# Optimization experiments

Measured on AMD Instinct MI355X. Metric: run time of the kernel, lower is better.

## Reference

```python
import jax, jax.numpy as jnp
import numpy as np

D_MODEL = 1024
NUM_HEADS = 16
HEAD_DIM = D_MODEL // NUM_HEADS  # 64
ROPE_THETA = 10000.0
SEQ_LEN = 4096
BATCH = 1


def apply_rope(x, positions, theta=ROPE_THETA):
    # x: [b, h, s, d], positions: [s]
    d = x.shape[-1]
    inv_freq = theta ** (-jnp.arange(0, d, 2, dtype=jnp.float32) / d)  # [d/2]
    angles = positions.astype(jnp.float32)[:, None] * inv_freq[None, :]  # [s, d/2]
    cos = jnp.cos(angles)  # [s, d/2]
    sin = jnp.sin(angles)
    x1 = x[..., 0::2]  # [b, h, s, d/2]
    x2 = x[..., 1::2]
    r1 = x1 * cos - x2 * sin
    r2 = x1 * sin + x2 * cos
    # interleave back to [..., d]
    out = jnp.stack([r1, r2], axis=-1).reshape(x.shape)
    return out.astype(x.dtype)


def setup_inputs() -> dict:
    key = jax.random.key(0)
    k_x, k_qkv, k_o = jax.random.split(key, 3)
    scale_in = 1.0 / np.sqrt(D_MODEL)
    return {
        "x": jax.random.normal(k_x, (BATCH, SEQ_LEN, D_MODEL), dtype=jnp.float32),
        "token_positions": jnp.arange(SEQ_LEN, dtype=jnp.int64 if jax.config.jax_enable_x64 else jnp.int32),
        "w_qkv": jax.random.normal(k_qkv, (3 * D_MODEL, D_MODEL), dtype=jnp.float32) * scale_in,
        "w_o": jax.random.normal(k_o, (D_MODEL, D_MODEL), dtype=jnp.float32) * scale_in,
    }


def reference(x, token_positions, w_qkv, w_o):
    b, s, _ = x.shape
    # QKV projection (Linear without bias, weight [out, in])
    x_qkv = jnp.einsum('bsd,ed->bse', x, w_qkv)  # [b, s, 3*d_model]
    # rearrange 'b s (three heads kv) -> three b heads s kv'
    x_qkv = x_qkv.reshape(b, s, 3, NUM_HEADS, HEAD_DIM)
    x_qkv = jnp.transpose(x_qkv, (2, 0, 3, 1, 4))  # [3, b, h, s, d]
    q, k, v = x_qkv[0], x_qkv[1], x_qkv[2]
    q = apply_rope(q, token_positions)
    k = apply_rope(k, token_positions)
    # scaled dot-product attention with causal mask
    scores = jnp.einsum('bhnd,bhmd->bhnm', q, k) / jnp.sqrt(jnp.float32(HEAD_DIM))
    causal = jnp.tril(jnp.ones((s, s), dtype=bool))  # [s, s]
    scores = jnp.where(causal[None, None], scores, jnp.float32(-jnp.inf))
    weights = jax.nn.softmax(scores, axis=-1)
    attn = jnp.einsum('bhnm,bhmd->bhnd', weights, v)  # [b, h, s, d]
    attn = jnp.transpose(attn, (0, 2, 1, 3)).reshape(b, s, NUM_HEADS * HEAD_DIM)
    return jnp.einsum('bsd,ed->bse', attn, w_o)
```

## Files before the change

kernel.cpp:

```cpp
#include <hip/hip_runtime.h>

#define SEQ 4096
#define DMODEL 1024
#define HEADS 16
#define HD 64
#define NQKV 3072

typedef __attribute__((ext_vector_type(8))) __bf16 bf16x8;
typedef __attribute__((ext_vector_type(4))) __bf16 bf16x4;
typedef __attribute__((ext_vector_type(8))) short short8;
typedef __attribute__((ext_vector_type(4))) float f32x4;
typedef __attribute__((ext_vector_type(16))) float f32x16;
typedef __attribute__((ext_vector_type(4))) unsigned int u32x4;

__device__ __forceinline__ unsigned short f2bf(float f) {
    unsigned u = __builtin_bit_cast(unsigned, f);
    return (unsigned short)((u + 0x7fffu + ((u >> 16) & 1u)) >> 16);
}
__device__ __forceinline__ float bf2f(unsigned short h) {
    return __builtin_bit_cast(float, (unsigned)h << 16);
}
__device__ __forceinline__ unsigned cvt_pk_bf16(float lo, float hi) {
    unsigned r;
    asm("v_cvt_pk_bf16_f32 %0, %1, %2" : "=v"(r) : "v"(lo), "v"(hi));
    return r;
}

__device__ __forceinline__ void gload16(const void* g, void* l) {
    __builtin_amdgcn_global_load_lds(
        (const __attribute__((address_space(1))) unsigned int*)g,
        (__attribute__((address_space(3))) unsigned int*)l, 16, 0, 0);
}

#define TS(qt, kh) (0x40 | ((kh) << 5) | (qt))
__device__ __constant__ unsigned char TASKS[48] = {
    TS(31,0), TS(31,1), TS(30,0), 15,
    TS(30,1), TS(29,0), TS(29,1), TS(28,0), 14,
    TS(28,1), TS(27,0), TS(27,1), TS(26,0), 13,
    TS(26,1), TS(25,0), TS(25,1), TS(24,0), 12,
    TS(24,1), TS(23,0), TS(23,1), TS(22,0), 11,
    TS(22,1), TS(21,0), TS(21,1), TS(20,0), 10,
    TS(20,1), TS(19,0), TS(19,1), TS(18,0), 9,
    TS(18,1), TS(17,0), TS(17,1), TS(16,0), 8,
    TS(16,1), 7,
    6, 5, 4, 3, 2, 1, 0
};

__global__ void f2bf_all(const float* __restrict__ x, const float* __restrict__ wqkv,
                         const float* __restrict__ wo, unsigned short* __restrict__ dst) {
    const int N0 = SEQ * DMODEL / 4;
    const int N1 = N0 + NQKV * DMODEL / 4;
    const int NT = N1 + DMODEL * DMODEL / 4;
    int i = blockIdx.x * 256 + threadIdx.x;
    int stride = gridDim.x * 256;
    for (; i < NT; i += stride) {
        const float4* src;
        if (i < N0)      src = reinterpret_cast<const float4*>(x) + i;
        else if (i < N1) src = reinterpret_cast<const float4*>(wqkv) + (i - N0);
        else             src = reinterpret_cast<const float4*>(wo) + (i - N1);
        float4 f = *src;
        ushort4 o;
        o.x = f2bf(f.x); o.y = f2bf(f.y); o.z = f2bf(f.z); o.w = f2bf(f.w);
        reinterpret_cast<ushort4*>(dst)[i] = o;
    }
}

template <int EPI>
__global__ __launch_bounds__(256) void gemm_bt(const unsigned short* __restrict__ A,
                                               const unsigned short* __restrict__ B,
                                               float* __restrict__ outF,
                                               unsigned short* __restrict__ outB,
                                               int M, int N, int K) {
    alignas(16) __shared__ unsigned short a_lds[2][128 * 32];
    alignas(16) __shared__ unsigned short b_lds[2][128 * 32];
    const int tid = threadIdx.x;
    const int wave = tid >> 6, lane = tid & 63;
    const int l16 = lane & 15, g = lane >> 4;
    const int wr = wave >> 1, wc = wave & 1;
    const int bm = blockIdx.x, bn = blockIdx.y;

    const int lrow = lane >> 2;
    const int lcol = (lane & 3) * 8;

    const unsigned short* Ag = A + (size_t)(bm * 128 + lrow) * K + lcol;
    const unsigned short* Bg = B + (size_t)(bn * 128 + lrow) * K + lcol;

    f32x4 acc[4][4] = {};
    const int NS = K / 32;

    auto STAGE = [&](int b, int ks) {
#pragma unroll
        for (int j = 0; j < 2; ++j) {
            int chunk = wave * 2 + j;
            gload16(Ag + (size_t)(chunk * 16) * K + ks * 32, a_lds[b] + chunk * 512);
            gload16(Bg + (size_t)(chunk * 16) * K + ks * 32, b_lds[b] + chunk * 512);
        }
    };

    STAGE(0, 0);

    for (int ks = 0; ks < NS; ++ks) {
        const int cur = ks & 1;
        asm volatile("s_waitcnt vmcnt(0)" ::: "memory");
        __builtin_amdgcn_s_barrier();
        if (ks + 1 < NS) STAGE(cur ^ 1, ks + 1);

        bf16x8 af[4], bfr[4];
#pragma unroll
        for (int m = 0; m < 4; ++m)
            af[m] = *reinterpret_cast<const bf16x8*>(a_lds[cur] + (wr * 64 + m * 16 + l16) * 32 + g * 8);
#pragma unroll
        for (int n = 0; n < 4; ++n)
            bfr[n] = *reinterpret_cast<const bf16x8*>(b_lds[cur] + (wc * 64 + n * 16 + l16) * 32 + g * 8);
        __builtin_amdgcn_s_setprio(1);
#pragma unroll
        for (int m = 0; m < 4; ++m)
#pragma unroll
            for (int n = 0; n < 4; ++n)
                acc[m][n] = __builtin_amdgcn_mfma_f32_16x16x32_bf16(af[m], bfr[n], acc[m][n], 0, 0, 0);
        __builtin_amdgcn_s_setprio(0);
    }

#pragma unroll
    for (int m = 0; m < 4; ++m)
#pragma unroll
        for (int n = 0; n < 4; ++n)
#pragma unroll
            for (int r = 0; r < 4; ++r) {
                int row = bm * 128 + wr * 64 + m * 16 + g * 4 + r;
                int col = bn * 128 + wc * 64 + n * 16 + l16;
                float v = acc[m][n][r];
                if (EPI == 0) {
                    int part = col >> 10;
                    int hd = col & 1023;
                    int h = hd >> 6, d = hd & 63;
                    outB[(size_t)((part * HEADS + h) * SEQ + row) * HD + d] = f2bf(v);
                } else {
                    outF[(size_t)row * N + col] = v;
                }
            }
}

__global__ __launch_bounds__(256) void rope_kernel(unsigned short* qkv, const int* __restrict__ pos) {
    int idx = blockIdx.x * 256 + threadIdx.x;
    int chunk = idx & 7;
    int row = idx >> 3;
    int s = row & (SEQ - 1);
    int ph = row >> 12;
    float p = (float)pos[s];
    float scale = (ph < HEADS) ? 0.125f * 1.4426950408889634f : 1.0f;
    unsigned short* base = qkv + ((size_t)ph * SEQ + s) * HD + chunk * 8;
    short8 v = *reinterpret_cast<short8*>(base);
    short8 o;
    const float k = -13.287712379549449f / 32.0f;
#pragma unroll
    for (int j = 0; j < 4; ++j) {
        int i = chunk * 4 + j;
        float ang = p * exp2f((float)i * k);
        float sn, cs;
        sincosf(ang, &sn, &cs);
        float x1 = bf2f((unsigned short)v[2 * j]);
        float x2 = bf2f((unsigned short)v[2 * j + 1]);
        o[2 * j]     = (short)f2bf((x1 * cs - x2 * sn) * scale);
        o[2 * j + 1] = (short)f2bf((x1 * sn + x2 * cs) * scale);
    }
    *reinterpret_cast<short8*>(base) = o;
}

__global__ __launch_bounds__(256) void transpose_v(const unsigned short* __restrict__ qkv,
                                                   unsigned short* __restrict__ vt) {
    const int st = blockIdx.x;
    const int h = blockIdx.y;
    __shared__ unsigned short tile[64][72];
    const unsigned short* Vg = qkv + (size_t)((2 * HEADS + h) * SEQ) * HD;
    const int tid = threadIdx.x;
#pragma unroll
    for (int j = 0; j < 2; ++j) {
        int b = (tid + j * 256) * 8;
        int row = b >> 6;
        int col = b & 63;
        short8 v = *reinterpret_cast<const short8*>(Vg + (size_t)(st * 64 + row) * HD + col);
#pragma unroll
        for (int i = 0; i < 8; ++i) tile[row][col + i] = (unsigned short)v[i];
    }
    __syncthreads();
#pragma unroll
    for (int j = 0; j < 2; ++j) {
        int b = (tid + j * 256) * 8;
        int d = b >> 6;
        int sc = b & 63;
        short8 o;
#pragma unroll
        for (int i = 0; i < 8; ++i) o[i] = (short)tile[sc + i][d];
        *reinterpret_cast<short8*>(vt + (size_t)(h * HD + d) * SEQ + st * 64 + sc) = o;
    }
}

__global__ __launch_bounds__(256) void attn_kernel(const unsigned short* __restrict__ qkv,
                                                   const unsigned short* __restrict__ vt,
                                                   unsigned short* __restrict__ attnout,
                                                   unsigned short* __restrict__ pO,
                                                   float* __restrict__ lmf) {
    const int bid = blockIdx.x;
    const int xcd = bid & 7;
    const int slot = bid >> 3;
    const int hloc = slot & 1;
    const unsigned char e = TASKS[slot >> 1];
    const int qtile = e & 31;
    const int khalf = (e >> 5) & 1;
    const bool isSplit = (e >> 6) != 0;
    const int T = qtile + 1, Hh = (T + 1) >> 1;
    const int k0 = isSplit ? (khalf ? Hh : 0) : 0;
    const int k1 = isSplit ? (khalf ? T : Hh) : T;
    const int h = xcd * 2 + hloc;

    const int tid = threadIdx.x;
    const int wave = tid >> 6, lane = tid & 63;
    const int l32 = lane & 31, hi = lane >> 5;

    alignas(16) __shared__ unsigned short k_lds[2][128 * 64];
    alignas(16) __shared__ unsigned short v_lds[2][2][64 * 64];

    const unsigned short* Qg = qkv + (size_t)((0 * HEADS + h) * SEQ) * HD;
    const unsigned short* Kg = qkv + (size_t)((1 * HEADS + h) * SEQ) * HD;
    const unsigned short* VTg = vt + (size_t)h * HD * SEQ;

    const int qbase = qtile * 128 + wave * 32;
    const int qrow = qbase + l32;

    bf16x8 qf[4];
#pragma unroll
    for (int dg = 0; dg < 4; ++dg)
        qf[dg] = *reinterpret_cast<const bf16x8*>(Qg + (size_t)qrow * HD + dg * 16 + hi * 8);

    f32x16 oa[2] = {};
    float m_r = -1e30f, l_r = 0.f;

    const int rsw = (l32 & 7) << 4;

    auto STAGE = [&](int b, int kt) {
#pragma unroll
        for (int i = 0; i < 4; ++i) {
            int base = wave * 4096 + i * 1024;
            int byte = base + lane * 16;
            int krow = byte >> 7;
            int kc8 = ((byte >> 4) & 7) ^ (krow & 7);
            gload16(Kg + (size_t)(kt * 128 + krow) * HD + kc8 * 8, (char*)k_lds[b] + base);
            int fr = byte >> 7;
            int h64 = fr >> 6, vd = fr & 63;
            int vc8 = ((byte >> 4) & 7) ^ (vd & 7);
            gload16(VTg + (size_t)vd * SEQ + kt * 128 + h64 * 64 + vc8 * 8,
                    (char*)v_lds[b] + base);
        }
    };

    STAGE(0, k0);

    for (int kt = k0; kt < k1; ++kt) {
        const int cur = (kt - k0) & 1;
        asm volatile("s_waitcnt vmcnt(0)" ::: "memory");
        __builtin_amdgcn_s_barrier();
        if (kt + 1 < k1) STAGE(cur ^ 1, kt + 1);

#pragma unroll
        for (int hh = 0; hh < 2; ++hh) {
            if (hh && (kt * 128 + 64) > (qbase + 31)) break;

            f32x16 s[2] = {};
            __builtin_amdgcn_s_setprio(1);
#pragma unroll
            for (int g = 0; g < 2; ++g) {
                int row = hh * 64 + g * 32 + l32;
#pragma unroll
                for (int dg = 0; dg < 4; ++dg) {
                    bf16x8 kf = *reinterpret_cast<const bf16x8*>(
                        (char*)k_lds[cur] + row * 128 + ((dg * 32 + hi * 16) ^ rsw));
                    s[g] = __builtin_amdgcn_mfma_f32_32x32x16_bf16(kf, qf[dg], s[g], 0, 0, 0);
                }
            }
            __builtin_amdgcn_s_setprio(0);

            if (kt * 128 + hh * 64 + 63 > qbase) {
#pragma unroll
                for (int g = 0; g < 2; ++g)
#pragma unroll
                    for (int r = 0; r < 16; ++r) {
                        int kv = kt * 128 + hh * 64 + g * 32 + (r & 3) + 8 * (r >> 2) + 4 * hi;
                        if (kv > qrow) s[g][r] = -1e30f;
                    }
            }

            float ma = -1e30f, mb = -1e30f, mc = -1e30f, md = -1e30f;
#pragma unroll
            for (int r = 0; r < 16; r += 4) {
                ma = fmaxf(ma, fmaxf(s[0][r], s[1][r]));
                mb = fmaxf(mb, fmaxf(s[0][r + 1], s[1][r + 1]));
                mc = fmaxf(mc, fmaxf(s[0][r + 2], s[1][r + 2]));
                md = fmaxf(md, fmaxf(s[0][r + 3], s[1][r + 3]));
            }
            float mx = fmaxf(fmaxf(ma, mb), fmaxf(mc, md));
            mx = fmaxf(mx, __shfl_xor(mx, 32));

            if (__any(mx > m_r + 8.0f)) {
                float mnew = fmaxf(m_r, mx);
                float alpha = __builtin_amdgcn_exp2f(m_r - mnew);
                m_r = mnew;
#pragma unroll
                for (int r = 0; r < 16; ++r) { oa[0][r] *= alpha; oa[1][r] *= alpha; }
                l_r *= alpha;
            }

#pragma unroll
            for (int g = 0; g < 2; ++g)
#pragma unroll
                for (int r = 0; r < 16; ++r) s[g][r] = __builtin_amdgcn_exp2f(s[g][r] - m_r);

            float ra = 0.f, rb = 0.f;
#pragma unroll
            for (int r = 0; r < 16; r += 2) {
                ra += s[0][r] + s[1][r];
                rb += s[0][r + 1] + s[1][r + 1];
            }
            float rs = ra + rb;
            rs += __shfl_xor(rs, 32);
            l_r += rs;

            __builtin_amdgcn_s_setprio(1);
#pragma unroll
            for (int g = 0; g < 2; ++g) {
                u32x4 pfw[2];
#pragma unroll
                for (int u = 0; u < 2; ++u) {
                    unsigned wA = cvt_pk_bf16(s[g][8 * u + 0], s[g][8 * u + 1]);
                    unsigned wC = cvt_pk_bf16(s[g][8 * u + 2], s[g][8 * u + 3]);
                    unsigned wB = cvt_pk_bf16(s[g][8 * u + 4], s[g][8 * u + 5]);
                    unsigned wD = cvt_pk_bf16(s[g][8 * u + 6], s[g][8 * u + 7]);
                    unsigned wAx = __shfl_xor((int)wA, 32), wBx = __shfl_xor((int)wB, 32);
                    unsigned wCx = __shfl_xor((int)wC, 32), wDx = __shfl_xor((int)wD, 32);
                    pfw[u][0] = hi ? wBx : wA;
                    pfw[u][1] = hi ? wDx : wC;
                    pfw[u][2] = hi ? wB : wAx;
                    pfw[u][3] = hi ? wD : wCx;
                }
#pragma unroll
                for (int u = 0; u < 2; ++u) {
                    bf16x8 pf = __builtin_bit_cast(bf16x8, pfw[u]);
                    int ks = g * 2 + u;
#pragma unroll
                    for (int dg = 0; dg < 2; ++dg) {
                        bf16x8 vf = *reinterpret_cast<const bf16x8*>(
                            (char*)v_lds[cur][hh] + (dg * 32 + l32) * 128 + ((ks * 32 + hi * 16) ^ rsw));
                        oa[dg] = __builtin_amdgcn_mfma_f32_32x32x16_bf16(vf, pf, oa[dg], 0, 0, 0);
                    }
                }
            }
            __builtin_amdgcn_s_setprio(0);
        }
    }

    const int ql = wave * 32 + l32;
    if (isSplit) {
        int sidx = (h * 16 + (qtile - 16)) * 2 + khalf;
        unsigned short* Op = pO + (size_t)sidx * 8192;
#pragma unroll
        for (int dg = 0; dg < 2; ++dg)
#pragma unroll
            for (int rq = 0; rq < 4; ++rq) {
                ushort4 ov;
                ov.x = f2bf(oa[dg][4 * rq + 0]);
                ov.y = f2bf(oa[dg][4 * rq + 1]);
                ov.z = f2bf(oa[dg][4 * rq + 2]);
                ov.w = f2bf(oa[dg][4 * rq + 3]);
                *reinterpret_cast<ushort4*>(Op + ql * 64 + dg * 32 + 8 * rq + 4 * hi) = ov;
            }
        if (hi == 0) {
            lmf[sidx * 256 + ql] = l_r;
            lmf[sidx * 256 + 128 + ql] = m_r;
        }
    } else {
        float inv = 1.0f / l_r;
        unsigned short* orow = attnout + (size_t)(qtile * 128 + ql) * DMODEL + h * HD;
#pragma unroll
        for (int dg = 0; dg < 2; ++dg)
#pragma unroll
            for (int rq = 0; rq < 4; ++rq) {
                ushort4 ov;
                ov.x = f2bf(oa[dg][4 * rq + 0] * inv);
                ov.y = f2bf(oa[dg][4 * rq + 1] * inv);
                ov.z = f2bf(oa[dg][4 * rq + 2] * inv);
                ov.w = f2bf(oa[dg][4 * rq + 3] * inv);
                *reinterpret_cast<ushort4*>(orow + dg * 32 + 8 * rq + 4 * hi) = ov;
            }
    }
}

__global__ __launch_bounds__(256) void merge_kernel(const unsigned short* __restrict__ pO,
                                                    const float* __restrict__ lmf,
                                                    unsigned short* __restrict__ attnout) {
    int idx = blockIdx.x * 256 + threadIdx.x;
    if (idx >= 16 * 16 * 1024) return;
    int h = idx / (16 * 1024);
    int r = idx % (16 * 1024);
    int qt = r >> 10;
    int rr = r & 1023;
    int q = rr >> 3, d8 = rr & 7;

    int s0 = (h * 16 + qt) * 2;
    float l0 = lmf[s0 * 256 + q],       m0 = lmf[s0 * 256 + 128 + q];
    float l1 = lmf[(s0 + 1) * 256 + q], m1 = lmf[(s0 + 1) * 256 + 128 + q];
    float m = fmaxf(m0, m1);
    float a0 = __builtin_amdgcn_exp2f(m0 - m), a1 = __builtin_amdgcn_exp2f(m1 - m);
    float L = l0 * a0 + l1 * a1;
    float c0 = a0 / L, c1 = a1 / L;

    const unsigned short* O0 = pO + (size_t)s0 * 8192 + q * 64 + d8 * 8;
    const unsigned short* O1 = O0 + 8192;
    short8 v0 = *reinterpret_cast<const short8*>(O0);
    short8 v1 = *reinterpret_cast<const short8*>(O1);
    short8 o;
#pragma unroll
    for (int j = 0; j < 8; ++j) {
        float val = bf2f((unsigned short)v0[j]) * c0 + bf2f((unsigned short)v1[j]) * c1;
        o[j] = (short)f2bf(val);
    }
    int qtile = qt + 16;
    *reinterpret_cast<short8*>(attnout + (size_t)(qtile * 128 + q) * DMODEL + h * HD + d8 * 8) = o;
}

extern "C" void kernel_launch(void* const* d_in, const int* in_sizes, int n_in,
                              void* d_out, int out_size, void* d_ws, size_t ws_size,
                              hipStream_t stream) {
    const float* x = (const float*)d_in[0];
    const int* pos = (const int*)d_in[1];
    const float* wqkv = (const float*)d_in[2];
    const float* wo = (const float*)d_in[3];
    float* out = (float*)d_out;

    unsigned short* xb = (unsigned short*)d_ws;
    unsigned short* wqkvb = xb + (size_t)SEQ * DMODEL;
    unsigned short* wob = wqkvb + (size_t)NQKV * DMODEL;
    unsigned short* qkvp = wob + (size_t)DMODEL * DMODEL;
    unsigned short* vt = qkvp + (size_t)3 * HEADS * SEQ * HD;
    unsigned short* attnb = vt + (size_t)HEADS * HD * SEQ;

    char* sbase = (char*)d_ws;
    float* lmf = (float*)sbase;
    unsigned short* pO = (unsigned short*)(sbase + (1 << 20));

    f2bf_all<<<2048, 256, 0, stream>>>(x, wqkv, wo, xb);

    dim3 g1(SEQ / 128, NQKV / 128);
    gemm_bt<0><<<g1, 256, 0, stream>>>(xb, wqkvb, nullptr, qkvp, SEQ, NQKV, DMODEL);

    rope_kernel<<<(2 * HEADS * SEQ * 8) / 256, 256, 0, stream>>>(qkvp, pos);
    transpose_v<<<dim3(SEQ / 64, HEADS), 256, 0, stream>>>(qkvp, vt);

    attn_kernel<<<768, 256, 0, stream>>>(qkvp, vt, attnb, pO, lmf);
    merge_kernel<<<(16 * 16 * 1024 + 255) / 256, 256, 0, stream>>>(pO, lmf, attnb);

    dim3 g2(SEQ / 128, DMODEL / 128);
    gemm_bt<1><<<g2, 256, 0, stream>>>(attnb, wob, out, nullptr, SEQ, DMODEL, DMODEL);
}
```

Before: 158.0 us.

## Use 256-row query tiles with persistent atomic work queue per XCD in attention

The attention kernel moves from 128-row query tiles with 256 threads to 256-row tiles with 512 threads (8 waves). The static one-block-per-task grid becomes persistent blocks that pull tasks from a per-XCD atomic counter, with a new split/unsplit task table and a matching merge kernel. The intent is better load balance across the causal triangle and more K/V reuse per staged tile, at the cost of extra barriers per task, a memset launch, and higher register/LDS pressure per block.

```diff
diff --git a/kernel.cpp b/kernel.cpp
--- a/kernel.cpp
+++ b/kernel.cpp
@@ -33,17 +33,12 @@
 }
 
 #define TS(qt, kh) (0x40 | ((kh) << 5) | (qt))
-__device__ __constant__ unsigned char TASKS[48] = {
-    TS(31,0), TS(31,1), TS(30,0), 15,
-    TS(30,1), TS(29,0), TS(29,1), TS(28,0), 14,
-    TS(28,1), TS(27,0), TS(27,1), TS(26,0), 13,
-    TS(26,1), TS(25,0), TS(25,1), TS(24,0), 12,
-    TS(24,1), TS(23,0), TS(23,1), TS(22,0), 11,
-    TS(22,1), TS(21,0), TS(21,1), TS(20,0), 10,
-    TS(20,1), TS(19,0), TS(19,1), TS(18,0), 9,
-    TS(18,1), TS(17,0), TS(17,1), TS(16,0), 8,
-    TS(16,1), 7,
-    6, 5, 4, 3, 2, 1, 0
+__device__ __constant__ unsigned char TASKS[28] = {
+    TS(15,0), TS(15,1), TS(14,0), TS(14,1), TS(13,0), TS(13,1),
+    TS(12,0), TS(12,1), TS(11,0), TS(11,1), TS(10,0), TS(10,1),
+    TS(9,0),  TS(9,1),  TS(8,0),  TS(8,1),  TS(7,0),  TS(7,1),
+    3,        TS(6,0),  TS(6,1),  2,        TS(5,0),  TS(5,1),
+    TS(4,0),  TS(4,1),  1,        0
 };
 
 __global__ void f2bf_all(const float* __restrict__ x, const float* __restrict__ wqkv,
@@ -196,201 +191,209 @@
     }
 }
 
-__global__ __launch_bounds__(256) void attn_kernel(const unsigned short* __restrict__ qkv,
+__global__ __launch_bounds__(512) void attn_kernel(const unsigned short* __restrict__ qkv,
                                                    const unsigned short* __restrict__ vt,
                                                    unsigned short* __restrict__ attnout,
+                                                   int* __restrict__ qcnt,
                                                    unsigned short* __restrict__ pO,
                                                    float* __restrict__ lmf) {
-    const int bid = blockIdx.x;
-    const int xcd = bid & 7;
-    const int slot = bid >> 3;
-    const int hloc = slot & 1;
-    const unsigned char e = TASKS[slot >> 1];
-    const int qtile = e & 31;
-    const int khalf = (e >> 5) & 1;
-    const bool isSplit = (e >> 6) != 0;
-    const int T = qtile + 1, Hh = (T + 1) >> 1;
-    const int k0 = isSplit ? (khalf ? Hh : 0) : 0;
-    const int k1 = isSplit ? (khalf ? T : Hh) : T;
-    const int h = xcd * 2 + hloc;
-
+    const int xcd = blockIdx.x & 7;
     const int tid = threadIdx.x;
     const int wave = tid >> 6, lane = tid & 63;
     const int l32 = lane & 31, hi = lane >> 5;
 
     alignas(16) __shared__ unsigned short k_lds[2][128 * 64];
     alignas(16) __shared__ unsigned short v_lds[2][2][64 * 64];
-
-    const unsigned short* Qg = qkv + (size_t)((0 * HEADS + h) * SEQ) * HD;
-    const unsigned short* Kg = qkv + (size_t)((1 * HEADS + h) * SEQ) * HD;
-    const unsigned short* VTg = vt + (size_t)h * HD * SEQ;
-
-    const int qbase = qtile * 128 + wave * 32;
-    const int qrow = qbase + l32;
-
-    bf16x8 qf[4];
-#pragma unroll
-    for (int dg = 0; dg < 4; ++dg)
-        qf[dg] = *reinterpret_cast<const bf16x8*>(Qg + (size_t)qrow * HD + dg * 16 + hi * 8);
-
-    f32x16 oa[2] = {};
-    float m_r = -1e30f, l_r = 0.f;
+    __shared__ int slot_sh;
 
     const int rsw = (l32 & 7) << 4;
 
-    auto STAGE = [&](int b, int kt) {
-#pragma unroll
-        for (int i = 0; i < 4; ++i) {
-            int base = wave * 4096 + i * 1024;
-            int byte = base + lane * 16;
-            int krow = byte >> 7;
-            int kc8 = ((byte >> 4) & 7) ^ (krow & 7);
-            gload16(Kg + (size_t)(kt * 128 + krow) * HD + kc8 * 8, (char*)k_lds[b] + base);
-            int fr = byte >> 7;
-            int h64 = fr >> 6, vd = fr & 63;
-            int vc8 = ((byte >> 4) & 7) ^ (vd & 7);
-            gload16(VTg + (size_t)vd * SEQ + kt * 128 + h64 * 64 + vc8 * 8,
-                    (char*)v_lds[b] + base);
+    for (;;) {
+        if (tid == 0) slot_sh = atomicAdd(&qcnt[xcd], 1);
+        __syncthreads();
+        const int t = slot_sh;
+        __syncthreads();
+        if (t >= 56) break;
+
+        const int hloc = t & 1;
+        const unsigned char e = TASKS[t >> 1];
+        const int qtile = e & 31;
+        const int khalf = (e >> 5) & 1;
+        const bool isSplit = (e >> 6) != 0;
+        const int T = 2 * qtile + 2, Hh = qtile + 1;
+        const int k0 = isSplit ? (khalf ? Hh : 0) : 0;
+        const int k1 = isSplit ? (khalf ? T : Hh) : T;
+        const int h = xcd * 2 + hloc;
+
+        const unsigned short* Qg = qkv + (size_t)((0 * HEADS + h) * SEQ) * HD;
+        const unsigned short* Kg = qkv + (size_t)((1 * HEADS + h) * SEQ) * HD;
+        const unsigned short* VTg = vt + (size_t)h * HD * SEQ;
+
+        const int qbase = qtile * 256 + wave * 32;
+        const int qrow = qbase + l32;
+
+        bf16x8 qf[4];
+#pragma unroll
+        for (int dg = 0; dg < 4; ++dg)
+            qf[dg] = *reinterpret_cast<const bf16x8*>(Qg + (size_t)qrow * HD + dg * 16 + hi * 8);
+
+        f32x16 oa[2] = {};
+        float m_r = -1e30f, l_r = 0.f;
+
+        auto STAGE = [&](int b, int kt) {
+#pragma unroll
+            for (int i = 0; i < 2; ++i) {
+                int base = wave * 2048 + i * 1024;
+                int byte = base + lane * 16;
+                int krow = byte >> 7;
+                int kc8 = ((byte >> 4) & 7) ^ (krow & 7);
+                gload16(Kg + (size_t)(kt * 128 + krow) * HD + kc8 * 8, (char*)k_lds[b] + base);
+                int fr = byte >> 7;
+                int h64 = fr >> 6, vd = fr & 63;
+                int vc8 = ((byte >> 4) & 7) ^ (vd & 7);
+                gload16(VTg + (size_t)vd * SEQ + kt * 128 + h64 * 64 + vc8 * 8,
+                        (char*)v_lds[b] + base);
+            }
+        };
+
+        STAGE(0, k0);
+
+        for (int kt = k0; kt < k1; ++kt) {
+            const int cur = (kt - k0) & 1;
+            asm volatile("s_waitcnt vmcnt(0)" ::: "memory");
+            __builtin_amdgcn_s_barrier();
+            if (kt + 1 < k1) STAGE(cur ^ 1, kt + 1);
+
+#pragma unroll
+            for (int hh = 0; hh < 2; ++hh) {
+                if (hh && (kt * 128 + 64) > (qbase + 31)) break;
+
+                f32x16 s[2] = {};
+                __builtin_amdgcn_s_setprio(1);
+#pragma unroll
+                for (int g = 0; g < 2; ++g) {
+                    int row = hh * 64 + g * 32 + l32;
+#pragma unroll
+                    for (int dg = 0; dg < 4; ++dg) {
+                        bf16x8 kf = *reinterpret_cast<const bf16x8*>(
+                            (char*)k_lds[cur] + row * 128 + ((dg * 32 + hi * 16) ^ rsw));
+                        s[g] = __builtin_amdgcn_mfma_f32_32x32x16_bf16(kf, qf[dg], s[g], 0, 0, 0);
+                    }
+                }
+                __builtin_amdgcn_s_setprio(0);
+
+                if (kt * 128 + hh * 64 + 63 > qbase) {
+#pragma unroll
+                    for (int g = 0; g < 2; ++g)
+#pragma unroll
+                        for (int r = 0; r < 16; ++r) {
+                            int kv = kt * 128 + hh * 64 + g * 32 + (r & 3) + 8 * (r >> 2) + 4 * hi;
+                            if (kv > qrow) s[g][r] = -1e30f;
+                        }
+                }
+
+                float ma = -1e30f, mb = -1e30f, mc = -1e30f, md = -1e30f;
+#pragma unroll
+                for (int r = 0; r < 16; r += 4) {
+                    ma = fmaxf(ma, fmaxf(s[0][r], s[1][r]));
+                    mb = fmaxf(mb, fmaxf(s[0][r + 1], s[1][r + 1]));
+                    mc = fmaxf(mc, fmaxf(s[0][r + 2], s[1][r + 2]));
+                    md = fmaxf(md, fmaxf(s[0][r + 3], s[1][r + 3]));
+                }
+                float mx = fmaxf(fmaxf(ma, mb), fmaxf(mc, md));
+                mx = fmaxf(mx, __shfl_xor(mx, 32));
+
+                if (__any(mx > m_r + 8.0f)) {
+                    float mnew = fmaxf(m_r, mx);
+                    float alpha = __builtin_amdgcn_exp2f(m_r - mnew);
+                    m_r = mnew;
+#pragma unroll
+                    for (int r = 0; r < 16; ++r) { oa[0][r] *= alpha; oa[1][r] *= alpha; }
+                    l_r *= alpha;
+                }
+
+#pragma unroll
+                for (int g = 0; g < 2; ++g)
+#pragma unroll
+                    for (int r = 0; r < 16; ++r) s[g][r] = __builtin_amdgcn_exp2f(s[g][r] - m_r);
+
+                float ra = 0.f, rb = 0.f;
+#pragma unroll
+                for (int r = 0; r < 16; r += 2) {
+                    ra += s[0][r] + s[1][r];
+                    rb += s[0][r + 1] + s[1][r + 1];
+                }
+                float rs = ra + rb;
+                rs += __shfl_xor(rs, 32);
+                l_r += rs;
+
+                __builtin_amdgcn_s_setprio(1);
+#pragma unroll
+                for (int g = 0; g < 2; ++g) {
+                    u32x4 pfw[2];
+#pragma unroll
+                    for (int u = 0; u < 2; ++u) {
+                        unsigned wA = cvt_pk_bf16(s[g][8 * u + 0], s[g][8 * u + 1]);
+                        unsigned wC = cvt_pk_bf16(s[g][8 * u + 2], s[g][8 * u + 3]);
+                        unsigned wB = cvt_pk_bf16(s[g][8 * u + 4], s[g][8 * u + 5]);
+                        unsigned wD = cvt_pk_bf16(s[g][8 * u + 6], s[g][8 * u + 7]);
+                        unsigned wAx = __shfl_xor((int)wA, 32), wBx = __shfl_xor((int)wB, 32);
+                        unsigned wCx = __shfl_xor((int)wC, 32), wDx = __shfl_xor((int)wD, 32);
+                        pfw[u][0] = hi ? wBx : wA;
+                        pfw[u][1] = hi ? wDx : wC;
+                        pfw[u][2] = hi ? wB : wAx;
+                        pfw[u][3] = hi ? wD : wCx;
+                    }
+#pragma unroll
+                    for (int u = 0; u < 2; ++u) {
+                        bf16x8 pf = __builtin_bit_cast(bf16x8, pfw[u]);
+                        int ks = g * 2 + u;
+#pragma unroll
+                        for (int dg = 0; dg < 2; ++dg) {
+                            bf16x8 vf = *reinterpret_cast<const bf16x8*>(
+                                (char*)v_lds[cur][hh] + (dg * 32 + l32) * 128 + ((ks * 32 + hi * 16) ^ rsw));
+                            oa[dg] = __builtin_amdgcn_mfma_f32_32x32x16_bf16(vf, pf, oa[dg], 0, 0, 0);
+                        }
+                    }
+                }
+                __builtin_amdgcn_s_setprio(0);
+            }
         }
-    };
-
-    STAGE(0, k0);
-
-    for (int kt = k0; kt < k1; ++kt) {
-        const int cur = (kt - k0) & 1;
-        asm volatile("s_waitcnt vmcnt(0)" ::: "memory");
-        __builtin_amdgcn_s_barrier();
-        if (kt + 1 < k1) STAGE(cur ^ 1, kt + 1);
-
-#pragma unroll
-        for (int hh = 0; hh < 2; ++hh) {
-            if (hh && (kt * 128 + 64) > (qbase + 31)) break;
-
-            f32x16 s[2] = {};
-            __builtin_amdgcn_s_setprio(1);
-#pragma unroll
-            for (int g = 0; g < 2; ++g) {
-                int row = hh * 64 + g * 32 + l32;
-#pragma unroll
-                for (int dg = 0; dg < 4; ++dg) {
-                    bf16x8 kf = *reinterpret_cast<const bf16x8*>(
-                        (char*)k_lds[cur] + row * 128 + ((dg * 32 + hi * 16) ^ rsw));
-                    s[g] = __builtin_amdgcn_mfma_f32_32x32x16_bf16(kf, qf[dg], s[g], 0, 0, 0);
-                }
+
+        const int ql = wave * 32 + l32;
+        if (isSplit) {
+            int sidx = (h * 12 + (qtile - 4)) * 2 + khalf;
+            unsigned short* Op = pO + (size_t)sidx * 16384;
+#pragma unroll
+            for (int dg = 0; dg < 2; ++dg)
+#pragma unroll
+                for (int rq = 0; rq < 4; ++rq) {
+                    ushort4 ov;
+                    ov.x = f2bf(oa[dg][4 * rq + 0]);
+                    ov.y = f2bf(oa[dg][4 * rq + 1]);
+                    ov.z = f2bf(oa[dg][4 * rq + 2]);
+                    ov.w = f2bf(oa[dg][4 * rq + 3]);
+                    *reinterpret_cast<ushort4*>(Op + ql * 64 + dg * 32 + 8 * rq + 4 * hi) = ov;
+                }
+            if (hi == 0) {
+                lmf[sidx * 512 + ql] = l_r;
+                lmf[sidx * 512 + 256 + ql] = m_r;
             }
-            __builtin_amdgcn_s_setprio(0);
-
-            if (kt * 128 + hh * 64 + 63 > qbase) {
-#pragma unroll
-                for (int g = 0; g < 2; ++g)
-#pragma unroll
-                    for (int r = 0; r < 16; ++r) {
-                        int kv = kt * 128 + hh * 64 + g * 32 + (r & 3) + 8 * (r >> 2) + 4 * hi;
-                        if (kv > qrow) s[g][r] = -1e30f;
-                    }
-            }
-
-            float ma = -1e30f, mb = -1e30f, mc = -1e30f, md = -1e30f;
-#pragma unroll
-            for (int r = 0; r < 16; r += 4) {
-                ma = fmaxf(ma, fmaxf(s[0][r], s[1][r]));
-                mb = fmaxf(mb, fmaxf(s[0][r + 1], s[1][r + 1]));
-                mc = fmaxf(mc, fmaxf(s[0][r + 2], s[1][r + 2]));
-                md = fmaxf(md, fmaxf(s[0][r + 3], s[1][r + 3]));
-            }
-            float mx = fmaxf(fmaxf(ma, mb), fmaxf(mc, md));
-            mx = fmaxf(mx, __shfl_xor(mx, 32));
-
-            if (__any(mx > m_r + 8.0f)) {
-                float mnew = fmaxf(m_r, mx);
-                float alpha = __builtin_amdgcn_exp2f(m_r - mnew);
-                m_r = mnew;
-#pragma unroll
-                for (int r = 0; r < 16; ++r) { oa[0][r] *= alpha; oa[1][r] *= alpha; }
-                l_r *= alpha;
-            }
-
-#pragma unroll
-            for (int g = 0; g < 2; ++g)
-#pragma unroll
-                for (int r = 0; r < 16; ++r) s[g][r] = __builtin_amdgcn_exp2f(s[g][r] - m_r);
-
-            float ra = 0.f, rb = 0.f;
-#pragma unroll
-            for (int r = 0; r < 16; r += 2) {
-                ra += s[0][r] + s[1][r];
-                rb += s[0][r + 1] + s[1][r + 1];
-            }
-            float rs = ra + rb;
-            rs += __shfl_xor(rs, 32);
-            l_r += rs;
-
-            __builtin_amdgcn_s_setprio(1);
-#pragma unroll
-            for (int g = 0; g < 2; ++g) {
-                u32x4 pfw[2];
-#pragma unroll
-                for (int u = 0; u < 2; ++u) {
-                    unsigned wA = cvt_pk_bf16(s[g][8 * u + 0], s[g][8 * u + 1]);
-                    unsigned wC = cvt_pk_bf16(s[g][8 * u + 2], s[g][8 * u + 3]);
-                    unsigned wB = cvt_pk_bf16(s[g][8 * u + 4], s[g][8 * u + 5]);
-                    unsigned wD = cvt_pk_bf16(s[g][8 * u + 6], s[g][8 * u + 7]);
-                    unsigned wAx = __shfl_xor((int)wA, 32), wBx = __shfl_xor((int)wB, 32);
-                    unsigned wCx = __shfl_xor((int)wC, 32), wDx = __shfl_xor((int)wD, 32);
-                    pfw[u][0] = hi ? wBx : wA;
-                    pfw[u][1] = hi ? wDx : wC;
-                    pfw[u][2] = hi ? wB : wAx;
-                    pfw[u][3] = hi ? wD : wCx;
-                }
-#pragma unroll
-                for (int u = 0; u < 2; ++u) {
-                    bf16x8 pf = __builtin_bit_cast(bf16x8, pfw[u]);
-                    int ks = g * 2 + u;
-#pragma unroll
-                    for (int dg = 0; dg < 2; ++dg) {
-                        bf16x8 vf = *reinterpret_cast<const bf16x8*>(
-                            (char*)v_lds[cur][hh] + (dg * 32 + l32) * 128 + ((ks * 32 + hi * 16) ^ rsw));
-                        oa[dg] = __builtin_amdgcn_mfma_f32_32x32x16_bf16(vf, pf, oa[dg], 0, 0, 0);
-                    }
-                }
-            }
-            __builtin_amdgcn_s_setprio(0);
+        } else {
+            float inv = 1.0f / l_r;
+            unsigned short* orow = attnout + (size_t)(qtile * 256 + ql) * DMODEL + h * HD;
+#pragma unroll
+            for (int dg = 0; dg < 2; ++dg)
+#pragma unroll
+                for (int rq = 0; rq < 4; ++rq) {
+                    ushort4 ov;
+                    ov.x = f2bf(oa[dg][4 * rq + 0] * inv);
+                    ov.y = f2bf(oa[dg][4 * rq + 1] * inv);
+                    ov.z = f2bf(oa[dg][4 * rq + 2] * inv);
+                    ov.w = f2bf(oa[dg][4 * rq + 3] * inv);
+                    *reinterpret_cast<ushort4*>(orow + dg * 32 + 8 * rq + 4 * hi) = ov;
+                }
         }
-    }
-
-    const int ql = wave * 32 + l32;
-    if (isSplit) {
-        int sidx = (h * 16 + (qtile - 16)) * 2 + khalf;
-        unsigned short* Op = pO + (size_t)sidx * 8192;
-#pragma unroll
-        for (int dg = 0; dg < 2; ++dg)
-#pragma unroll
-            for (int rq = 0; rq < 4; ++rq) {
-                ushort4 ov;
-                ov.x = f2bf(oa[dg][4 * rq + 0]);
-                ov.y = f2bf(oa[dg][4 * rq + 1]);
-                ov.z = f2bf(oa[dg][4 * rq + 2]);
-                ov.w = f2bf(oa[dg][4 * rq + 3]);
-                *reinterpret_cast<ushort4*>(Op + ql * 64 + dg * 32 + 8 * rq + 4 * hi) = ov;
-            }
-        if (hi == 0) {
-            lmf[sidx * 256 + ql] = l_r;
-            lmf[sidx * 256 + 128 + ql] = m_r;
-        }
-    } else {
-        float inv = 1.0f / l_r;
-        unsigned short* orow = attnout + (size_t)(qtile * 128 + ql) * DMODEL + h * HD;
-#pragma unroll
-        for (int dg = 0; dg < 2; ++dg)
-#pragma unroll
-            for (int rq = 0; rq < 4; ++rq) {
-                ushort4 ov;
-                ov.x = f2bf(oa[dg][4 * rq + 0] * inv);
-                ov.y = f2bf(oa[dg][4 * rq + 1] * inv);
-                ov.z = f2bf(oa[dg][4 * rq + 2] * inv);
-                ov.w = f2bf(oa[dg][4 * rq + 3] * inv);
-                *reinterpret_cast<ushort4*>(orow + dg * 32 + 8 * rq + 4 * hi) = ov;
-            }
     }
 }
 
@@ -398,23 +401,23 @@
                                                     const float* __restrict__ lmf,
                                                     unsigned short* __restrict__ attnout) {
     int idx = blockIdx.x * 256 + threadIdx.x;
-    if (idx >= 16 * 16 * 1024) return;
-    int h = idx / (16 * 1024);
-    int r = idx % (16 * 1024);
-    int qt = r >> 10;
-    int rr = r & 1023;
+    if (idx >= 16 * 12 * 2048) return;
+    int h = idx / (12 * 2048);
+    int r = idx % (12 * 2048);
+    int qt = r >> 11;
+    int rr = r & 2047;
     int q = rr >> 3, d8 = rr & 7;
 
-    int s0 = (h * 16 + qt) * 2;
-    float l0 = lmf[s0 * 256 + q],       m0 = lmf[s0 * 256 + 128 + q];
-    float l1 = lmf[(s0 + 1) * 256 + q], m1 = lmf[(s0 + 1) * 256 + 128 + q];
+    int s0 = (h * 12 + qt) * 2;
+    float l0 = lmf[s0 * 512 + q],       m0 = lmf[s0 * 512 + 256 + q];
+    float l1 = lmf[(s0 + 1) * 512 + q], m1 = lmf[(s0 + 1) * 512 + 256 + q];
     float m = fmaxf(m0, m1);
     float a0 = __builtin_amdgcn_exp2f(m0 - m), a1 = __builtin_amdgcn_exp2f(m1 - m);
     float L = l0 * a0 + l1 * a1;
     float c0 = a0 / L, c1 = a1 / L;
 
-    const unsigned short* O0 = pO + (size_t)s0 * 8192 + q * 64 + d8 * 8;
-    const unsigned short* O1 = O0 + 8192;
+    const unsigned short* O0 = pO + (size_t)s0 * 16384 + q * 64 + d8 * 8;
+    const unsigned short* O1 = O0 + 16384;
     short8 v0 = *reinterpret_cast<const short8*>(O0);
     short8 v1 = *reinterpret_cast<const short8*>(O1);
     short8 o;
@@ -423,8 +426,8 @@
         float val = bf2f((unsigned short)v0[j]) * c0 + bf2f((unsigned short)v1[j]) * c1;
         o[j] = (short)f2bf(val);
     }
-    int qtile = qt + 16;
-    *reinterpret_cast<short8*>(attnout + (size_t)(qtile * 128 + q) * DMODEL + h * HD + d8 * 8) = o;
+    int qtile = qt + 4;
+    *reinterpret_cast<short8*>(attnout + (size_t)(qtile * 256 + q) * DMODEL + h * HD + d8 * 8) = o;
 }
 
 extern "C" void kernel_launch(void* const* d_in, const int* in_sizes, int n_in,
@@ -444,7 +447,8 @@
     unsigned short* attnb = vt + (size_t)HEADS * HD * SEQ;
 
     char* sbase = (char*)d_ws;
-    float* lmf = (float*)sbase;
+    int* qcnt = (int*)sbase;
+    float* lmf = (float*)(sbase + 1024);
     unsigned short* pO = (unsigned short*)(sbase + (1 << 20));
 
     f2bf_all<<<2048, 256, 0, stream>>>(x, wqkv, wo, xb);
@@ -455,8 +459,9 @@
     rope_kernel<<<(2 * HEADS * SEQ * 8) / 256, 256, 0, stream>>>(qkvp, pos);
     transpose_v<<<dim3(SEQ / 64, HEADS), 256, 0, stream>>>(qkvp, vt);
 
-    attn_kernel<<<768, 256, 0, stream>>>(qkvp, vt, attnb, pO, lmf);
-    merge_kernel<<<(16 * 16 * 1024 + 255) / 256, 256, 0, stream>>>(pO, lmf, attnb);
+    hipMemsetAsync(qcnt, 0, 64, stream);
+    attn_kernel<<<512, 512, 0, stream>>>(qkvp, vt, attnb, qcnt, pO, lmf);
+    merge_kernel<<<(16 * 12 * 2048 + 255) / 256, 256, 0, stream>>>(pO, lmf, attnb);
 
     dim3 g2(SEQ / 128, DMODEL / 128);
     gemm_bt<1><<<g2, 256, 0, stream>>>(attnb, wob, out, nullptr, SEQ, DMODEL, DMODEL);
```

Measured after the change: 147.2 us. 1.07x faster.
